# Kernel tuning notes

Measured on AMD Instinct MI355X. Metric: run time of the kernel, lower is better.

Reference implementation:

```python
import jax, jax.numpy as jnp
import numpy as np

NUM_USERS = 100000
NUM_ITEMS = 200000
N = NUM_USERS + NUM_ITEMS
E = 2000000
D = 64
N_LAYERS = 3


def setup_inputs() -> dict:
    key = jax.random.key(0)
    k1, k2, k3, k4, k5 = jax.random.split(key, 5)
    # Xavier-uniform-ish init (scale irrelevant for correctness baseline)
    user_emb = jax.random.normal(k1, (NUM_USERS, D), dtype=jnp.float32) * 0.1
    item_emb = jax.random.normal(k2, (NUM_ITEMS, D), dtype=jnp.float32) * 0.1
    adj_rows = jax.random.randint(k3, (E,), 0, N, dtype=jnp.int32)
    adj_cols = jax.random.randint(k4, (E,), 0, N, dtype=jnp.int32)
    # normalized adjacency values (D^-1/2 A D^-1/2 in real LightGCN); random positives here
    adj_vals = jax.random.uniform(k5, (E,), dtype=jnp.float32) * 0.1
    return {"user_emb": user_emb, "item_emb": item_emb,
            "adj_rows": adj_rows, "adj_cols": adj_cols, "adj_vals": adj_vals}


def _spmm(rows, cols, vals, x):
    # y[r] = sum over edges (r,c,v): v * x[c]   -- COO SpMM via gather + segment_sum
    gathered = x[cols] * vals[:, None]  # [E, D]
    return jax.ops.segment_sum(gathered, rows, num_segments=N)


def reference(user_emb, item_emb, adj_rows, adj_cols, adj_vals):
    ego = jnp.concatenate([user_emb, item_emb], axis=0)  # [N, D]
    acc = ego
    h = ego
    for _ in range(N_LAYERS):
        h = _spmm(adj_rows, adj_cols, adj_vals, h)
        acc = acc + h
    final = acc / jnp.float32(N_LAYERS + 1)  # mean over layer stack, fused
    return final[:NUM_USERS], final[NUM_USERS:]
```

## Files before the change

kernel.cpp:

```cpp
#include <hip/hip_runtime.h>
#include <hip/hip_bf16.h>


#define NUM_USERS 100000
#define NUM_ITEMS 200000
#define NN (NUM_USERS + NUM_ITEMS)
#define DIM 64
#define BROWS 1024
#define NB_BUCKETS ((NN + BROWS - 1) / BROWS)
#define CHUNK 4096
#define RK 16
#define OVF 4096

typedef unsigned short ushort8_t __attribute__((ext_vector_type(8)));

__device__ __forceinline__ float bf16_to_f32(unsigned short u) {
    return __uint_as_float(((unsigned int)u) << 16);
}
__device__ __forceinline__ unsigned short f32_to_bf16(float f) {
    unsigned int u = __float_as_uint(f);
    u += 0x7fffu + ((u >> 16) & 1u);
    return (unsigned short)(u >> 16);
}

__global__ void zero_ints(int* __restrict__ p, int n) {
    int i = blockIdx.x * blockDim.x + threadIdx.x;
    if (i < n) p[i] = 0;
}

__global__ void hist_kernel(const int* __restrict__ rows, int* __restrict__ counts, int E) {
    int e = blockIdx.x * blockDim.x + threadIdx.x;
    if (e < E) atomicAdd(&counts[rows[e]], 1);
}

__global__ void scan_partials(const int* __restrict__ counts, int* __restrict__ blocksums, int n) {
    __shared__ int lds[256];
    int tid = threadIdx.x;
    int base = blockIdx.x * 1024 + tid * 4;
    int s = 0;
#pragma unroll
    for (int k = 0; k < 4; ++k) { int idx = base + k; if (idx < n) s += counts[idx]; }
    lds[tid] = s;
    __syncthreads();
    for (int off = 128; off > 0; off >>= 1) {
        if (tid < off) lds[tid] += lds[tid + off];
        __syncthreads();
    }
    if (tid == 0) blocksums[blockIdx.x] = lds[0];
}

__global__ void scan_blocksums_par(int* __restrict__ blocksums, int nb,
                                   int* __restrict__ row_start, int n) {
    __shared__ int lds[512];
    int t = threadIdx.x;
    int v = (t < nb) ? blocksums[t] : 0;
    lds[t] = v;
    __syncthreads();
    for (int off = 1; off < 512; off <<= 1) {
        int u = (t >= off) ? lds[t - off] : 0;
        __syncthreads();
        lds[t] += u;
        __syncthreads();
    }
    if (t < nb) blocksums[t] = lds[t] - v;
    if (t == 0) row_start[n] = lds[nb - 1];
}

__global__ void scan_write(int* __restrict__ counts, const int* __restrict__ blocksums,
                           int* __restrict__ cursor, int n) {
    __shared__ int lds[256];
    int tid = threadIdx.x;
    int base = blockIdx.x * 1024 + tid * 4;
    int local[4]; int tsum = 0;
#pragma unroll
    for (int k = 0; k < 4; ++k) {
        int idx = base + k;
        local[k] = (idx < n) ? counts[idx] : 0;
        tsum += local[k];
    }
    lds[tid] = tsum;
    __syncthreads();
    for (int off = 1; off < 256; off <<= 1) {
        int v = 0;
        if (tid >= off) v = lds[tid - off];
        __syncthreads();
        lds[tid] += v;
        __syncthreads();
    }
    int run = lds[tid] - tsum + blocksums[blockIdx.x];
#pragma unroll
    for (int k = 0; k < 4; ++k) {
        int idx = base + k;
        if (idx < n) { counts[idx] = run; cursor[idx] = run; run += local[k]; }
    }
}

__global__ void init_bcur(const int* __restrict__ row_start, int* __restrict__ bcur) {
    int b = threadIdx.x;
    if (b < NB_BUCKETS) bcur[b] = row_start[b << 10];
}

__global__ __launch_bounds__(512) void bin_edges(const int* __restrict__ rows,
                                                 const int* __restrict__ cols,
                                                 const float* __restrict__ vals,
                                                 int* __restrict__ bcur,
                                                 uint2* __restrict__ epack, int E) {
    __shared__ int lcnt[512];
    __shared__ int lscan[512];
    __shared__ int lcur[512];
    __shared__ int gbase[512];
    __shared__ uint2 stage[CHUNK];
    __shared__ int dstg[CHUNK];

    int t = threadIdx.x;
    int base = blockIdx.x * CHUNK;
    int n = E - base; if (n > CHUNK) n = CHUNK;

    lcnt[t] = 0;
    __syncthreads();

    int r[8], c[8], b[8];
    unsigned int vb[8];
    int ebase = base + t * 8;
    if (ebase + 8 <= E) {
        int4 r0 = *(const int4*)(rows + ebase);
        int4 r1 = *(const int4*)(rows + ebase + 4);
        int4 c0 = *(const int4*)(cols + ebase);
        int4 c1 = *(const int4*)(cols + ebase + 4);
        float4 v0 = *(const float4*)(vals + ebase);
        float4 v1 = *(const float4*)(vals + ebase + 4);
        r[0]=r0.x; r[1]=r0.y; r[2]=r0.z; r[3]=r0.w; r[4]=r1.x; r[5]=r1.y; r[6]=r1.z; r[7]=r1.w;
        c[0]=c0.x; c[1]=c0.y; c[2]=c0.z; c[3]=c0.w; c[4]=c1.x; c[5]=c1.y; c[6]=c1.z; c[7]=c1.w;
        vb[0]=__float_as_uint(v0.x); vb[1]=__float_as_uint(v0.y);
        vb[2]=__float_as_uint(v0.z); vb[3]=__float_as_uint(v0.w);
        vb[4]=__float_as_uint(v1.x); vb[5]=__float_as_uint(v1.y);
        vb[6]=__float_as_uint(v1.z); vb[7]=__float_as_uint(v1.w);
#pragma unroll
        for (int k = 0; k < 8; ++k) b[k] = r[k] >> 10;
    } else {
#pragma unroll
        for (int k = 0; k < 8; ++k) {
            int e = ebase + k;
            if (e < E) { r[k] = rows[e]; c[k] = cols[e]; vb[k] = __float_as_uint(vals[e]); b[k] = r[k] >> 10; }
            else b[k] = -1;
        }
    }
#pragma unroll
    for (int k = 0; k < 8; ++k)
        if (b[k] >= 0) atomicAdd(&lcnt[b[k]], 1);
    __syncthreads();

    int val = lcnt[t];
    lscan[t] = val;
    __syncthreads();
    for (int off = 1; off < 512; off <<= 1) {
        int u = (t >= off) ? lscan[t - off] : 0;
        __syncthreads();
        lscan[t] += u;
        __syncthreads();
    }
    int excl = lscan[t] - val;
    lscan[t] = excl;
    lcur[t]  = excl;
    if (t < NB_BUCKETS && val > 0)
        gbase[t] = atomicAdd(&bcur[t], val);
    __syncthreads();

#pragma unroll
    for (int k = 0; k < 8; ++k) {
        int bb = b[k];
        if (bb >= 0) {
            int l = atomicAdd(&lcur[bb], 1);
            unsigned int w0 = (unsigned int)c[k] | (((unsigned int)(r[k] & (BROWS - 1))) << 19);
            stage[l] = make_uint2(w0, vb[k]);
            dstg[l] = gbase[bb] + (l - lscan[bb]);
        }
    }
    __syncthreads();

    for (int l = t; l < n; l += 512)
        epack[dstg[l]] = stage[l];
}

__global__ __launch_bounds__(512) void bucket_scatter(const int* __restrict__ row_start,
                                                      uint2* __restrict__ epack) {
    __shared__ int cur[BROWS];
    __shared__ uint2 ovf[OVF];
    int b = blockIdx.x;
    int t = threadIdx.x;
    int rbase = b << 10;
    int rend = rbase + BROWS; if (rend > NN) rend = NN;
    int s = row_start[rbase];
    int e = row_start[rend];
    int cnt = e - s;

    for (int r = t; r < rend - rbase; r += 512)
        cur[r] = row_start[rbase + r];

    uint2 p[RK];
#pragma unroll
    for (int k = 0; k < RK; ++k) {
        int idx = t + k * 512;
        if (s + idx < e) p[k] = epack[s + idx];
    }
    for (int l = 8192 + t; l < cnt && l < 8192 + OVF; l += 512)
        ovf[l - 8192] = epack[s + l];
    __syncthreads();

#pragma unroll
    for (int k = 0; k < RK; ++k) {
        int idx = t + k * 512;
        if (s + idx < e) {
            uint2 w = p[k];
            int rl = (w.x >> 19) & (BROWS - 1);
            int pp = atomicAdd(&cur[rl], 1);
            epack[pp] = make_uint2(w.x & 0x7FFFFu, w.y);
        }
    }
    for (int l = 8192 + t; l < cnt && l < 8192 + OVF; l += 512) {
        uint2 w = ovf[l - 8192];
        int rl = (w.x >> 19) & (BROWS - 1);
        int pp = atomicAdd(&cur[rl], 1);
        epack[pp] = make_uint2(w.x & 0x7FFFFu, w.y);
    }
}

__global__ void init_h0(const float4* __restrict__ user4,
                        const float4* __restrict__ item4,
                        ushort4* __restrict__ h4,
                        int total4, int user4n) {
    int i = blockIdx.x * blockDim.x + threadIdx.x;
    if (i >= total4) return;
    float4 v = (i < user4n) ? user4[i] : item4[i - user4n];
    ushort4 b;
    b.x = f32_to_bf16(v.x); b.y = f32_to_bf16(v.y);
    b.z = f32_to_bf16(v.z); b.w = f32_to_bf16(v.w);
    h4[i] = b;
}

__global__ void spmm_gather(const int* __restrict__ row_start,
                            const float2* __restrict__ epack,
                            const unsigned short* __restrict__ x,
                            unsigned short* __restrict__ y) {
    int tid = threadIdx.x;
    int sub = tid >> 3;
    int lane = tid & 7;
    int row = blockIdx.x * 32 + sub;
    if (row >= NN) return;
    int s = row_start[row];
    int e = row_start[row + 1];
    int off = lane << 3;

    float a0[8], a1[8];
#pragma unroll
    for (int k = 0; k < 8; ++k) { a0[k] = 0.f; a1[k] = 0.f; }

    int j = s;
    for (; j + 1 < e; j += 2) {
        float2 e0 = epack[j];
        float2 e1 = epack[j + 1];
        int c0 = __float_as_int(e0.x);
        int c1 = __float_as_int(e1.x);
        ushort8_t x0 = *(const ushort8_t*)(x + c0 * DIM + off);
        ushort8_t x1 = *(const ushort8_t*)(x + c1 * DIM + off);
        float v0 = e0.y, v1 = e1.y;
#pragma unroll
        for (int k = 0; k < 8; ++k) a0[k] += v0 * bf16_to_f32(x0[k]);
#pragma unroll
        for (int k = 0; k < 8; ++k) a1[k] += v1 * bf16_to_f32(x1[k]);
    }
    if (j < e) {
        float2 e0 = epack[j];
        int c0 = __float_as_int(e0.x);
        ushort8_t x0 = *(const ushort8_t*)(x + c0 * DIM + off);
        float v0 = e0.y;
#pragma unroll
        for (int k = 0; k < 8; ++k) a0[k] += v0 * bf16_to_f32(x0[k]);
    }

    ushort8_t yb;
#pragma unroll
    for (int k = 0; k < 8; ++k) yb[k] = f32_to_bf16(a0[k] + a1[k]);
    *(ushort8_t*)(y + row * DIM + off) = yb;
}

__global__ void final_combine(const float4* __restrict__ user4,
                              const float4* __restrict__ item4,
                              const ushort4* __restrict__ h1,
                              const ushort4* __restrict__ h2,
                              const ushort4* __restrict__ h3,
                              float4* __restrict__ out4,
                              int total4, int user4n) {
    int i = blockIdx.x * blockDim.x + threadIdx.x;
    if (i >= total4) return;
    float4 ego = (i < user4n) ? user4[i] : item4[i - user4n];
    ushort4 a = h1[i], b = h2[i], c = h3[i];
    float4 o;
    o.x = (ego.x + bf16_to_f32(a.x) + bf16_to_f32(b.x) + bf16_to_f32(c.x)) * 0.25f;
    o.y = (ego.y + bf16_to_f32(a.y) + bf16_to_f32(b.y) + bf16_to_f32(c.y)) * 0.25f;
    o.z = (ego.z + bf16_to_f32(a.z) + bf16_to_f32(b.z) + bf16_to_f32(c.z)) * 0.25f;
    o.w = (ego.w + bf16_to_f32(a.w) + bf16_to_f32(b.w) + bf16_to_f32(c.w)) * 0.25f;
    out4[i] = o;
}

extern "C" void kernel_launch(void* const* d_in, const int* in_sizes, int n_in,
                              void* d_out, int out_size, void* d_ws, size_t ws_size,
                              hipStream_t stream) {
    const float* user_emb = (const float*)d_in[0];
    const float* item_emb = (const float*)d_in[1];
    const int*   adj_rows = (const int*)d_in[2];
    const int*   adj_cols = (const int*)d_in[3];
    const float* adj_vals = (const float*)d_in[4];
    float* out = (float*)d_out;

    const int E = in_sizes[2];
    const int total = NN * DIM;
    const int total4 = total / 4;
    const int user4n = NUM_USERS * DIM / 4;

    float2* epack = (float2*)d_ws;
    unsigned short* hA = (unsigned short*)(epack + E);
    unsigned short* hB = hA + total;
    unsigned short* hC = hB + total;
    int* row_start = (int*)(hC + total);
    int* cursor    = row_start + NN + 1;
    int* blocksums = cursor + NN + 1;

    const int TB = 256;
    const int gridV = (total4 + TB - 1) / TB;
    const int gridN = (NN + 1 + TB - 1) / TB;
    const int gridE = (E + TB - 1) / TB;
    const int nScan = (NN + 1023) / 1024;
    const int gridG = (NN + 31) / 32;
    const int nChunksA = (E + CHUNK - 1) / CHUNK;

    zero_ints<<<gridN, TB, 0, stream>>>(row_start, NN + 1);
    hist_kernel<<<gridE, TB, 0, stream>>>(adj_rows, row_start, E);
    scan_partials<<<nScan, TB, 0, stream>>>(row_start, blocksums, NN);
    scan_blocksums_par<<<1, 512, 0, stream>>>(blocksums, nScan, row_start, NN);
    scan_write<<<nScan, TB, 0, stream>>>(row_start, blocksums, cursor, NN);
    init_bcur<<<1, 512, 0, stream>>>(row_start, cursor);
    bin_edges<<<nChunksA, 512, 0, stream>>>(adj_rows, adj_cols, adj_vals, cursor,
                                            (uint2*)epack, E);
    bucket_scatter<<<NB_BUCKETS, 512, 0, stream>>>(row_start, (uint2*)epack);

    init_h0<<<gridV, TB, 0, stream>>>((const float4*)user_emb, (const float4*)item_emb,
                                      (ushort4*)hA, total4, user4n);

    spmm_gather<<<gridG, TB, 0, stream>>>(row_start, epack, hA, hB);
    spmm_gather<<<gridG, TB, 0, stream>>>(row_start, epack, hB, hC);
    spmm_gather<<<gridG, TB, 0, stream>>>(row_start, epack, hC, hA);

    final_combine<<<gridV, TB, 0, stream>>>((const float4*)user_emb, (const float4*)item_emb,
                                            (const ushort4*)hB, (const ushort4*)hC,
                                            (const ushort4*)hA, (float4*)out,
                                            total4, user4n);
}
```

Baseline: 452.2 us.

## Replace per-row histogram and global scan with bucket-level histogram and in-block row scan

Drops the per-row global atomic histogram over all edges and the three-kernel prefix scan across all rows. Instead, a per-chunk LDS histogram counts edges per 1024-row bucket and a single small scan produces bucket offsets. Each bucket_scatter block then counts its own rows in LDS, scans them, and writes row_start for its range. This cuts global atomics and several kernel launches, at the cost of extra LDS work and one more block-wide scan inside bucket_scatter.

```diff
diff --git a/kernel.cpp b/kernel.cpp
--- a/kernel.cpp
+++ b/kernel.cpp
@@ -28,32 +28,35 @@
     if (i < n) p[i] = 0;
 }
 
-__global__ void hist_kernel(const int* __restrict__ rows, int* __restrict__ counts, int E) {
-    int e = blockIdx.x * blockDim.x + threadIdx.x;
-    if (e < E) atomicAdd(&counts[rows[e]], 1);
-}
-
-__global__ void scan_partials(const int* __restrict__ counts, int* __restrict__ blocksums, int n) {
-    __shared__ int lds[256];
-    int tid = threadIdx.x;
-    int base = blockIdx.x * 1024 + tid * 4;
-    int s = 0;
-#pragma unroll
-    for (int k = 0; k < 4; ++k) { int idx = base + k; if (idx < n) s += counts[idx]; }
-    lds[tid] = s;
-    __syncthreads();
-    for (int off = 128; off > 0; off >>= 1) {
-        if (tid < off) lds[tid] += lds[tid + off];
-        __syncthreads();
-    }
-    if (tid == 0) blocksums[blockIdx.x] = lds[0];
-}
-
-__global__ void scan_blocksums_par(int* __restrict__ blocksums, int nb,
-                                   int* __restrict__ row_start, int n) {
+__global__ __launch_bounds__(512) void bucket_hist(const int* __restrict__ rows,
+                                                   int* __restrict__ bcnt, int E) {
+    __shared__ int h[512];
+    int t = threadIdx.x;
+    h[t] = 0;
+    __syncthreads();
+    int base = blockIdx.x * CHUNK + t * 8;
+    if (base + 8 <= E) {
+        int4 r0 = *(const int4*)(rows + base);
+        int4 r1 = *(const int4*)(rows + base + 4);
+        atomicAdd(&h[r0.x >> 10], 1); atomicAdd(&h[r0.y >> 10], 1);
+        atomicAdd(&h[r0.z >> 10], 1); atomicAdd(&h[r0.w >> 10], 1);
+        atomicAdd(&h[r1.x >> 10], 1); atomicAdd(&h[r1.y >> 10], 1);
+        atomicAdd(&h[r1.z >> 10], 1); atomicAdd(&h[r1.w >> 10], 1);
+    } else {
+        for (int k = 0; k < 8; ++k) {
+            int e = base + k;
+            if (e < E) atomicAdd(&h[rows[e] >> 10], 1);
+        }
+    }
+    __syncthreads();
+    if (t < NB_BUCKETS && h[t] > 0) atomicAdd(&bcnt[t], h[t]);
+}
+
+__global__ void scan_buckets(const int* __restrict__ bcnt, int* __restrict__ bbase,
+                             int* __restrict__ bcur, int* __restrict__ row_start, int E) {
     __shared__ int lds[512];
     int t = threadIdx.x;
-    int v = (t < nb) ? blocksums[t] : 0;
+    int v = bcnt[t];
     lds[t] = v;
     __syncthreads();
     for (int off = 1; off < 512; off <<= 1) {
@@ -62,42 +65,10 @@
         lds[t] += u;
         __syncthreads();
     }
-    if (t < nb) blocksums[t] = lds[t] - v;
-    if (t == 0) row_start[n] = lds[nb - 1];
-}
-
-__global__ void scan_write(int* __restrict__ counts, const int* __restrict__ blocksums,
-                           int* __restrict__ cursor, int n) {
-    __shared__ int lds[256];
-    int tid = threadIdx.x;
-    int base = blockIdx.x * 1024 + tid * 4;
-    int local[4]; int tsum = 0;
-#pragma unroll
-    for (int k = 0; k < 4; ++k) {
-        int idx = base + k;
-        local[k] = (idx < n) ? counts[idx] : 0;
-        tsum += local[k];
-    }
-    lds[tid] = tsum;
-    __syncthreads();
-    for (int off = 1; off < 256; off <<= 1) {
-        int v = 0;
-        if (tid >= off) v = lds[tid - off];
-        __syncthreads();
-        lds[tid] += v;
-        __syncthreads();
-    }
-    int run = lds[tid] - tsum + blocksums[blockIdx.x];
-#pragma unroll
-    for (int k = 0; k < 4; ++k) {
-        int idx = base + k;
-        if (idx < n) { counts[idx] = run; cursor[idx] = run; run += local[k]; }
-    }
-}
-
-__global__ void init_bcur(const int* __restrict__ row_start, int* __restrict__ bcur) {
-    int b = threadIdx.x;
-    if (b < NB_BUCKETS) bcur[b] = row_start[b << 10];
+    int base = lds[t] - v;
+    if (t <= NB_BUCKETS) bbase[t] = base;
+    if (t < NB_BUCKETS)  bcur[t] = base;
+    if (t == 0) row_start[NN] = E;
 }
 
 __global__ __launch_bounds__(512) void bin_edges(const int* __restrict__ rows,
@@ -182,35 +153,62 @@
         epack[dstg[l]] = stage[l];
 }
 
-__global__ __launch_bounds__(512) void bucket_scatter(const int* __restrict__ row_start,
+__global__ __launch_bounds__(512) void bucket_scatter(const int* __restrict__ bbase,
+                                                      int* __restrict__ row_start,
                                                       uint2* __restrict__ epack) {
     __shared__ int cur[BROWS];
+    __shared__ int stmp[512];
     __shared__ uint2 ovf[OVF];
     int b = blockIdx.x;
     int t = threadIdx.x;
     int rbase = b << 10;
-    int rend = rbase + BROWS; if (rend > NN) rend = NN;
-    int s = row_start[rbase];
-    int e = row_start[rend];
+    int nrows = NN - rbase; if (nrows > BROWS) nrows = BROWS;
+    int s = bbase[b];
+    int e = bbase[b + 1];
     int cnt = e - s;
 
-    for (int r = t; r < rend - rbase; r += 512)
-        cur[r] = row_start[rbase + r];
+    cur[t] = 0; cur[t + 512] = 0;
+    __syncthreads();
 
     uint2 p[RK];
 #pragma unroll
     for (int k = 0; k < RK; ++k) {
         int idx = t + k * 512;
-        if (s + idx < e) p[k] = epack[s + idx];
-    }
-    for (int l = 8192 + t; l < cnt && l < 8192 + OVF; l += 512)
-        ovf[l - 8192] = epack[s + l];
+        if (idx < cnt) {
+            p[k] = epack[s + idx];
+            atomicAdd(&cur[(p[k].x >> 19) & (BROWS - 1)], 1);
+        }
+    }
+    for (int l = 8192 + t; l < cnt && l < 8192 + OVF; l += 512) {
+        uint2 w = epack[s + l];
+        ovf[l - 8192] = w;
+        atomicAdd(&cur[(w.x >> 19) & (BROWS - 1)], 1);
+    }
+    __syncthreads();
+
+    int c0 = cur[2 * t], c1 = cur[2 * t + 1];
+    int ps = c0 + c1;
+    stmp[t] = ps;
+    __syncthreads();
+    for (int off = 1; off < 512; off <<= 1) {
+        int u = (t >= off) ? stmp[t - off] : 0;
+        __syncthreads();
+        stmp[t] += u;
+        __syncthreads();
+    }
+    int pexcl = stmp[t] - ps;
+    int b0 = s + pexcl;
+    int b1 = b0 + c0;
+    cur[2 * t] = b0;
+    cur[2 * t + 1] = b1;
+    if (2 * t < nrows)     row_start[rbase + 2 * t]     = b0;
+    if (2 * t + 1 < nrows) row_start[rbase + 2 * t + 1] = b1;
     __syncthreads();
 
 #pragma unroll
     for (int k = 0; k < RK; ++k) {
         int idx = t + k * 512;
-        if (s + idx < e) {
+        if (idx < cnt) {
             uint2 w = p[k];
             int rl = (w.x >> 19) & (BROWS - 1);
             int pp = atomicAdd(&cur[rl], 1);
@@ -323,26 +321,21 @@
     unsigned short* hB = hA + total;
     unsigned short* hC = hB + total;
     int* row_start = (int*)(hC + total);
-    int* cursor    = row_start + NN + 1;
-    int* blocksums = cursor + NN + 1;
+    int* bcnt  = row_start + NN + 1;
+    int* bbase = bcnt + 512;
+    int* bcur  = bbase + 512;
 
     const int TB = 256;
     const int gridV = (total4 + TB - 1) / TB;
-    const int gridN = (NN + 1 + TB - 1) / TB;
-    const int gridE = (E + TB - 1) / TB;
-    const int nScan = (NN + 1023) / 1024;
     const int gridG = (NN + 31) / 32;
     const int nChunksA = (E + CHUNK - 1) / CHUNK;
 
-    zero_ints<<<gridN, TB, 0, stream>>>(row_start, NN + 1);
-    hist_kernel<<<gridE, TB, 0, stream>>>(adj_rows, row_start, E);
-    scan_partials<<<nScan, TB, 0, stream>>>(row_start, blocksums, NN);
-    scan_blocksums_par<<<1, 512, 0, stream>>>(blocksums, nScan, row_start, NN);
-    scan_write<<<nScan, TB, 0, stream>>>(row_start, blocksums, cursor, NN);
-    init_bcur<<<1, 512, 0, stream>>>(row_start, cursor);
-    bin_edges<<<nChunksA, 512, 0, stream>>>(adj_rows, adj_cols, adj_vals, cursor,
+    zero_ints<<<1, 512, 0, stream>>>(bcnt, 512);
+    bucket_hist<<<nChunksA, 512, 0, stream>>>(adj_rows, bcnt, E);
+    scan_buckets<<<1, 512, 0, stream>>>(bcnt, bbase, bcur, row_start, E);
+    bin_edges<<<nChunksA, 512, 0, stream>>>(adj_rows, adj_cols, adj_vals, bcur,
                                             (uint2*)epack, E);
-    bucket_scatter<<<NB_BUCKETS, 512, 0, stream>>>(row_start, (uint2*)epack);
+    bucket_scatter<<<NB_BUCKETS, 512, 0, stream>>>(bbase, row_start, (uint2*)epack);
 
     init_h0<<<gridV, TB, 0, stream>>>((const float4*)user_emb, (const float4*)item_emb,
                                       (ushort4*)hA, total4, user4n);
```

Result: faster. 383.9 us (-15.1%).
